# Kernel tuning notes

Measured on AMD Instinct MI355X. Metric: run time of the kernel, lower is better.

The kernel has to match this reference:

```python
import jax, jax.numpy as jnp
import numpy as np

ELEM, EMBD, WIN = 128, 128, 128

def setup_inputs() -> dict:
    key = jax.random.key(0)
    ks = jax.random.split(key, 7)
    s = 1.0 / np.sqrt(ELEM)
    return {
        "x": jax.random.normal(ks[0], (8, 16384, ELEM), dtype=jnp.float32),
        "Wq": jax.random.uniform(ks[1], (EMBD, ELEM), jnp.float32, -s, s),
        "bq": jax.random.uniform(ks[2], (EMBD,), jnp.float32, -s, s),
        "Wk": jax.random.uniform(ks[3], (EMBD, ELEM), jnp.float32, -s, s),
        "bk": jax.random.uniform(ks[4], (EMBD,), jnp.float32, -s, s),
        "Wv": jax.random.uniform(ks[5], (EMBD, ELEM), jnp.float32, -s, s),
        "bv": jax.random.uniform(ks[6], (EMBD,), jnp.float32, -s, s),
    }

def reference(x, Wq, bq, Wk, bk, Wv, bv):
    N, S, E = x.shape
    P = S // WIN
    xp = x.reshape(N, P, WIN, E)  # [N,P,W,E]
    q = jnp.einsum('npwe,de->npwd', xp, Wq) + bq
    k = jnp.einsum('npwe,de->npwd', xp, Wk) + bk
    v = jnp.einsum('npwe,de->npwd', xp, Wv) + bv
    # note: original applies NO 1/sqrt(d) scaling
    scores = jnp.einsum('npwd,npud->npwu', q, k)  # [N,P,W,W]
    attn = jax.nn.softmax(scores, axis=-1)
    out = jnp.einsum('npwu,npud->npwd', attn, v)
    return out.reshape(N, S, EMBD)
```

## Files before the change

kernel.cpp:

```cpp
#include <hip/hip_runtime.h>

#define LDSP 136

typedef _Float16 h8 __attribute__((ext_vector_type(8)));
typedef _Float16 h4 __attribute__((ext_vector_type(4)));
typedef float    f4 __attribute__((ext_vector_type(4)));
typedef float    fx16 __attribute__((ext_vector_type(16)));
typedef unsigned u32x4 __attribute__((ext_vector_type(4)));

union VF { u32x4 u; h8 h; };

__device__ __forceinline__ void bar_lds() {
    asm volatile("s_waitcnt lgkmcnt(0)" ::: "memory");
    __builtin_amdgcn_s_barrier();
    __builtin_amdgcn_sched_barrier(0);
}

__device__ __forceinline__ unsigned pkh(float a, float b) {
    union { _Float16 h[2]; unsigned u; } t;
    t.h[0] = (_Float16)a; t.h[1] = (_Float16)b;
    return t.u;
}

__global__ void prep(const float* __restrict__ Wq, const float* __restrict__ Wk,
                     const float* __restrict__ bq, const float* __restrict__ Wv,
                     _Float16* __restrict__ Mt, _Float16* __restrict__ Wvh,
                     float* __restrict__ ck) {
    int idx = blockIdx.x * 256 + threadIdx.x;
    int e = idx & 127, f = idx >> 7;
    float a0 = 0.f, a1 = 0.f, a2 = 0.f, a3 = 0.f;
    for (int d = 0; d < 128; d += 4) {
        a0 += Wk[(d + 0) * 128 + f] * Wq[(d + 0) * 128 + e];
        a1 += Wk[(d + 1) * 128 + f] * Wq[(d + 1) * 128 + e];
        a2 += Wk[(d + 2) * 128 + f] * Wq[(d + 2) * 128 + e];
        a3 += Wk[(d + 3) * 128 + f] * Wq[(d + 3) * 128 + e];
    }
    Mt[idx]  = (_Float16)((a0 + a1) + (a2 + a3));
    Wvh[idx] = (_Float16)Wv[idx];

    if (blockIdx.x == 0 && threadIdx.x < 128) {
        int t = threadIdx.x;
        float c0 = 0.f, c1 = 0.f, c2 = 0.f, c3 = 0.f;
        for (int d = 0; d < 128; d += 4) {
            c0 += bq[d + 0] * Wk[(d + 0) * 128 + t];
            c1 += bq[d + 1] * Wk[(d + 1) * 128 + t];
            c2 += bq[d + 2] * Wk[(d + 2) * 128 + t];
            c3 += bq[d + 3] * Wk[(d + 3) * 128 + t];
        }
        ck[t] = (c0 + c1) + (c2 + c3);
    }
}

__global__ __launch_bounds__(512, 4) void attn(
    const float* __restrict__ x, const _Float16* __restrict__ Mt,
    const _Float16* __restrict__ Wvh, const float* __restrict__ ck,
    const float* __restrict__ bv, float* __restrict__ out) {
    __shared__ _Float16 Xs[128 * LDSP];
    __shared__ _Float16 Ts[128 * LDSP];
    __shared__ float2   Sm[256];

    const int tid  = threadIdx.x;
    const int wv   = tid >> 6;
    const int lane = tid & 63;
    const int l32  = lane & 31;
    const int hi   = lane >> 5;
    const int hv   = wv & 1;
    const int t4   = wv >> 1;

    const size_t base = (size_t)blockIdx.x * (128 * 128);

#pragma unroll
    for (int j = 0; j < 8; ++j) {
        int idx = 4 * tid + 2048 * j;
        int row = idx >> 7, col = idx & 127;
        f4 f = *(const f4*)(x + base + idx);
        h4 h = {(_Float16)f.x, (_Float16)f.y, (_Float16)f.z, (_Float16)f.w};
        *(h4*)(&Xs[row * LDSP + col]) = h;
    }
    bar_lds();

    const float bvv = bv[t4 * 32 + l32];

    VF vfr[8];
    {
        fx16 av0, av1, av2, av3;
#pragma unroll
        for (int r = 0; r < 16; ++r) av0[r] = bvv;
        av1 = av0; av2 = av0; av3 = av0;
#pragma unroll
        for (int e0 = 0; e0 < 8; ++e0) {
            h8 wf = *(const h8*)(Wvh + (t4 * 32 + l32) * 128 + e0 * 16 + hi * 8);
            h8 x0 = *(const h8*)(&Xs[( 0 + l32) * LDSP + e0 * 16 + hi * 8]);
            h8 x1 = *(const h8*)(&Xs[(32 + l32) * LDSP + e0 * 16 + hi * 8]);
            h8 x2 = *(const h8*)(&Xs[(64 + l32) * LDSP + e0 * 16 + hi * 8]);
            h8 x3 = *(const h8*)(&Xs[(96 + l32) * LDSP + e0 * 16 + hi * 8]);
            av0 = __builtin_amdgcn_mfma_f32_32x32x16_f16(x0, wf, av0, 0, 0, 0);
            av1 = __builtin_amdgcn_mfma_f32_32x32x16_f16(x1, wf, av1, 0, 0, 0);
            av2 = __builtin_amdgcn_mfma_f32_32x32x16_f16(x2, wf, av2, 0, 0, 0);
            av3 = __builtin_amdgcn_mfma_f32_32x32x16_f16(x3, wf, av3, 0, 0, 0);
        }
#define PACK_TILE(av, T) {                                                        \
        unsigned A0 = pkh(av[0], av[1]),  A1 = pkh(av[2], av[3]);                 \
        unsigned B0 = pkh(av[4], av[5]),  B1 = pkh(av[6], av[7]);                 \
        unsigned C0 = pkh(av[8], av[9]),  C1 = pkh(av[10], av[11]);               \
        unsigned D0 = pkh(av[12], av[13]), D1 = pkh(av[14], av[15]);              \
        asm volatile("v_permlane32_swap_b32 %0, %1" : "+v"(A0), "+v"(B0));        \
        asm volatile("v_permlane32_swap_b32 %0, %1" : "+v"(A1), "+v"(B1));        \
        asm volatile("v_permlane32_swap_b32 %0, %1" : "+v"(C0), "+v"(D0));        \
        asm volatile("v_permlane32_swap_b32 %0, %1" : "+v"(C1), "+v"(D1));        \
        vfr[2 * T].u     = (u32x4){A0, A1, B0, B1};                               \
        vfr[2 * T + 1].u = (u32x4){C0, C1, D0, D1};                               \
    }
        PACK_TILE(av0, 0) PACK_TILE(av1, 1) PACK_TILE(av2, 2) PACK_TILE(av3, 3)
#undef PACK_TILE
    }

    {
        fx16 accT0, accT1;
        {
            f4 ckv[4];
#pragma unroll
            for (int run = 0; run < 4; ++run)
                ckv[run] = *(const f4*)(ck + t4 * 32 + run * 8 + 4 * hi);
#pragma unroll
            for (int r = 0; r < 16; ++r) accT0[r] = ckv[r >> 2][r & 3];
            accT1 = accT0;
        }
#pragma unroll
        for (int e0 = 0; e0 < 8; ++e0) {
            h8 mt = *(const h8*)(Mt + (t4 * 32 + l32) * 128 + e0 * 16 + hi * 8);
            h8 b0 = *(const h8*)(&Xs[(hv * 64 + l32) * LDSP + e0 * 16 + hi * 8]);
            h8 b1 = *(const h8*)(&Xs[(hv * 64 + 32 + l32) * LDSP + e0 * 16 + hi * 8]);
            accT0 = __builtin_amdgcn_mfma_f32_32x32x16_f16(mt, b0, accT0, 0, 0, 0);
            accT1 = __builtin_amdgcn_mfma_f32_32x32x16_f16(mt, b1, accT1, 0, 0, 0);
        }
#pragma unroll
        for (int run = 0; run < 4; ++run) {
            h4 h0 = {(_Float16)accT0[run * 4 + 0], (_Float16)accT0[run * 4 + 1],
                     (_Float16)accT0[run * 4 + 2], (_Float16)accT0[run * 4 + 3]};
            *(h4*)(&Ts[(hv * 64 + l32) * LDSP + t4 * 32 + run * 8 + 4 * hi]) = h0;
            h4 h1 = {(_Float16)accT1[run * 4 + 0], (_Float16)accT1[run * 4 + 1],
                     (_Float16)accT1[run * 4 + 2], (_Float16)accT1[run * 4 + 3]};
            *(h4*)(&Ts[(hv * 64 + 32 + l32) * LDSP + t4 * 32 + run * 8 + 4 * hi]) = h1;
        }
    }
    bar_lds();

    fx16 s0, s1;
#pragma unroll
    for (int r = 0; r < 16; ++r) s0[r] = 0.f;
    s1 = s0;
#pragma unroll
    for (int f0 = 0; f0 < 8; ++f0) {
        h8 tf = *(const h8*)(&Ts[(t4 * 32 + l32) * LDSP + f0 * 16 + hi * 8]);
        h8 a0 = *(const h8*)(&Xs[(hv * 64 + l32) * LDSP + f0 * 16 + hi * 8]);
        h8 a1 = *(const h8*)(&Xs[(hv * 64 + 32 + l32) * LDSP + f0 * 16 + hi * 8]);
        s0 = __builtin_amdgcn_mfma_f32_32x32x16_f16(a0, tf, s0, 0, 0, 0);
        s1 = __builtin_amdgcn_mfma_f32_32x32x16_f16(a1, tf, s1, 0, 0, 0);
    }
    float m = -1e30f;
#pragma unroll
    for (int r = 0; r < 16; ++r) m = fmaxf(m, fmaxf(s0[r], s1[r]));
    m = fmaxf(m, __shfl_xor(m, 32, 64));
    float ss = 0.f;
#pragma unroll
    for (int r = 0; r < 16; ++r) {
        s0[r] = __expf(s0[r] - m);
        s1[r] = __expf(s1[r] - m);
        ss += s0[r] + s1[r];
    }
    ss += __shfl_xor(ss, 32, 64);
    if (hi == 0) Sm[hv * 128 + t4 * 32 + l32] = make_float2(m, ss);
    bar_lds();
    float2 om = Sm[(hv ^ 1) * 128 + t4 * 32 + l32];
    float M   = fmaxf(m, om.x);
    float inv = __expf(m - M) / (ss * __expf(m - M) + om.y * __expf(om.x - M));
#pragma unroll
    for (int run = 0; run < 4; ++run) {
        h4 p0 = {(_Float16)(s0[run * 4 + 0] * inv), (_Float16)(s0[run * 4 + 1] * inv),
                 (_Float16)(s0[run * 4 + 2] * inv), (_Float16)(s0[run * 4 + 3] * inv)};
        *(h4*)(&Ts[(t4 * 32 + l32) * LDSP + hv * 64 + run * 8 + 4 * hi]) = p0;
        h4 p1 = {(_Float16)(s1[run * 4 + 0] * inv), (_Float16)(s1[run * 4 + 1] * inv),
                 (_Float16)(s1[run * 4 + 2] * inv), (_Float16)(s1[run * 4 + 3] * inv)};
        *(h4*)(&Ts[(t4 * 32 + l32) * LDSP + hv * 64 + 32 + run * 8 + 4 * hi]) = p1;
    }
    bar_lds();

    fx16 o0, o1;
#pragma unroll
    for (int r = 0; r < 16; ++r) o0[r] = 0.f;
    o1 = o0;
#pragma unroll
    for (int us = 0; us < 8; ++us) {
        h8 p0 = *(const h8*)(&Ts[(hv * 32 + l32) * LDSP + us * 16 + hi * 8]);
        h8 p1 = *(const h8*)(&Ts[((2 + hv) * 32 + l32) * LDSP + us * 16 + hi * 8]);
        o0 = __builtin_amdgcn_mfma_f32_32x32x16_f16(p0, vfr[us].h, o0, 0, 0, 0);
        o1 = __builtin_amdgcn_mfma_f32_32x32x16_f16(p1, vfr[us].h, o1, 0, 0, 0);
    }
    float* ob = out + base;
#pragma unroll
    for (int r = 0; r < 16; ++r) {
        int wrow = (r & 3) + 8 * (r >> 2) + 4 * hi;
        ob[(size_t)(hv * 32 + wrow) * 128 + t4 * 32 + l32]       = o0[r];
        ob[(size_t)((2 + hv) * 32 + wrow) * 128 + t4 * 32 + l32] = o1[r];
    }
}

extern "C" void kernel_launch(void* const* d_in, const int* in_sizes, int n_in,
                              void* d_out, int out_size, void* d_ws, size_t ws_size,
                              hipStream_t stream) {
    const float* x  = (const float*)d_in[0];
    const float* Wq = (const float*)d_in[1];
    const float* bq = (const float*)d_in[2];
    const float* Wk = (const float*)d_in[3];
    const float* Wv = (const float*)d_in[5];
    const float* bv = (const float*)d_in[6];

    _Float16* Mt  = (_Float16*)d_ws;
    _Float16* Wvh = Mt + 16384;
    float*    ckp = (float*)(Wvh + 16384);

    prep<<<64, 256, 0, stream>>>(Wq, Wk, bq, Wv, Mt, Wvh, ckp);
    attn<<<1024, 512, 0, stream>>>(x, Mt, Wvh, ckp, bv, (float*)d_out);
}
```

Before: 146.5 us.

## Process four windows per block with register prefetch and in-register softmax

Each block now loops over four consecutive windows. It double-buffers the converted x tile in LDS and prefetches the next window's x into registers while the current one is computed. The wave decomposition changes so each wave owns whole score rows. Softmax then needs no cross-wave LDS reduction, and the T and P operands stay in registers via permlane packing, with V transposed into LDS instead. This removes barriers and LDS round trips, but the two waves sharing a row tile both compute the same projected-key and score tiles. The grid also shrinks to 256 blocks with launch bounds lowered to 2 blocks per SM.

```diff
diff --git a/kernel.cpp b/kernel.cpp
--- a/kernel.cpp
+++ b/kernel.cpp
@@ -20,6 +20,19 @@
     union { _Float16 h[2]; unsigned u; } t;
     t.h[0] = (_Float16)a; t.h[1] = (_Float16)b;
     return t.u;
+}
+
+#define PACK_TILE(av, out0, out1) {                                           \
+    unsigned A0 = pkh(av[0], av[1]),   A1 = pkh(av[2], av[3]);                \
+    unsigned B0 = pkh(av[4], av[5]),   B1 = pkh(av[6], av[7]);                \
+    unsigned C0 = pkh(av[8], av[9]),   C1 = pkh(av[10], av[11]);              \
+    unsigned D0 = pkh(av[12], av[13]), D1 = pkh(av[14], av[15]);              \
+    asm volatile("v_permlane32_swap_b32 %0, %1" : "+v"(A0), "+v"(B0));        \
+    asm volatile("v_permlane32_swap_b32 %0, %1" : "+v"(A1), "+v"(B1));        \
+    asm volatile("v_permlane32_swap_b32 %0, %1" : "+v"(C0), "+v"(D0));        \
+    asm volatile("v_permlane32_swap_b32 %0, %1" : "+v"(C1), "+v"(D1));        \
+    (out0).u = (u32x4){A0, A1, B0, B1};                                       \
+    (out1).u = (u32x4){C0, C1, D0, D1};                                       \
 }
 
 __global__ void prep(const float* __restrict__ Wq, const float* __restrict__ Wk,
@@ -51,158 +64,161 @@
     }
 }
 
-__global__ __launch_bounds__(512, 4) void attn(
+__global__ __launch_bounds__(512, 2) void attn(
     const float* __restrict__ x, const _Float16* __restrict__ Mt,
     const _Float16* __restrict__ Wvh, const float* __restrict__ ck,
     const float* __restrict__ bv, float* __restrict__ out) {
-    __shared__ _Float16 Xs[128 * LDSP];
-    __shared__ _Float16 Ts[128 * LDSP];
-    __shared__ float2   Sm[256];
+    __shared__ _Float16 Xs[2][128 * LDSP];
+    __shared__ _Float16 Vs[128 * LDSP];
 
     const int tid  = threadIdx.x;
     const int wv   = tid >> 6;
     const int lane = tid & 63;
     const int l32  = lane & 31;
     const int hi   = lane >> 5;
-    const int hv   = wv & 1;
-    const int t4   = wv >> 1;
-
-    const size_t base = (size_t)blockIdx.x * (128 * 128);
-
-#pragma unroll
-    for (int j = 0; j < 8; ++j) {
-        int idx = 4 * tid + 2048 * j;
-        int row = idx >> 7, col = idx & 127;
-        f4 f = *(const f4*)(x + base + idx);
-        h4 h = {(_Float16)f.x, (_Float16)f.y, (_Float16)f.z, (_Float16)f.w};
-        *(h4*)(&Xs[row * LDSP + col]) = h;
-    }
-    bar_lds();
-
-    const float bvv = bv[t4 * 32 + l32];
-
-    VF vfr[8];
-    {
-        fx16 av0, av1, av2, av3;
-#pragma unroll
-        for (int r = 0; r < 16; ++r) av0[r] = bvv;
-        av1 = av0; av2 = av0; av3 = av0;
-#pragma unroll
-        for (int e0 = 0; e0 < 8; ++e0) {
-            h8 wf = *(const h8*)(Wvh + (t4 * 32 + l32) * 128 + e0 * 16 + hi * 8);
-            h8 x0 = *(const h8*)(&Xs[( 0 + l32) * LDSP + e0 * 16 + hi * 8]);
-            h8 x1 = *(const h8*)(&Xs[(32 + l32) * LDSP + e0 * 16 + hi * 8]);
-            h8 x2 = *(const h8*)(&Xs[(64 + l32) * LDSP + e0 * 16 + hi * 8]);
-            h8 x3 = *(const h8*)(&Xs[(96 + l32) * LDSP + e0 * 16 + hi * 8]);
-            av0 = __builtin_amdgcn_mfma_f32_32x32x16_f16(x0, wf, av0, 0, 0, 0);
-            av1 = __builtin_amdgcn_mfma_f32_32x32x16_f16(x1, wf, av1, 0, 0, 0);
-            av2 = __builtin_amdgcn_mfma_f32_32x32x16_f16(x2, wf, av2, 0, 0, 0);
-            av3 = __builtin_amdgcn_mfma_f32_32x32x16_f16(x3, wf, av3, 0, 0, 0);
-        }
-#define PACK_TILE(av, T) {                                                        \
-        unsigned A0 = pkh(av[0], av[1]),  A1 = pkh(av[2], av[3]);                 \
-        unsigned B0 = pkh(av[4], av[5]),  B1 = pkh(av[6], av[7]);                 \
-        unsigned C0 = pkh(av[8], av[9]),  C1 = pkh(av[10], av[11]);               \
-        unsigned D0 = pkh(av[12], av[13]), D1 = pkh(av[14], av[15]);              \
-        asm volatile("v_permlane32_swap_b32 %0, %1" : "+v"(A0), "+v"(B0));        \
-        asm volatile("v_permlane32_swap_b32 %0, %1" : "+v"(A1), "+v"(B1));        \
-        asm volatile("v_permlane32_swap_b32 %0, %1" : "+v"(C0), "+v"(D0));        \
-        asm volatile("v_permlane32_swap_b32 %0, %1" : "+v"(C1), "+v"(D1));        \
-        vfr[2 * T].u     = (u32x4){A0, A1, B0, B1};                               \
-        vfr[2 * T + 1].u = (u32x4){C0, C1, D0, D1};                               \
-    }
-        PACK_TILE(av0, 0) PACK_TILE(av1, 1) PACK_TILE(av2, 2) PACK_TILE(av3, 3)
-#undef PACK_TILE
-    }
-
-    {
-        fx16 accT0, accT1;
+    const int wt   = wv >> 1;
+    const int ph   = wv & 1;
+
+    const float bvv = bv[wt * 32 + l32];
+    const size_t base0 = (size_t)blockIdx.x * 4 * (128 * 128);
+
+    f4 pf[8];
+#pragma unroll
+    for (int j = 0; j < 8; ++j)
+        pf[j] = *(const f4*)(x + base0 + 4 * tid + 2048 * j);
+
+    for (int it = 0; it < 4; ++it) {
+        _Float16* X = Xs[it & 1];
+
+#pragma unroll
+        for (int j = 0; j < 8; ++j) {
+            int idx = 4 * tid + 2048 * j;
+            int row = idx >> 7, col = idx & 127;
+            f4 f = pf[j];
+            h4 h = {(_Float16)f.x, (_Float16)f.y, (_Float16)f.z, (_Float16)f.w};
+            *(h4*)(&X[row * LDSP + col]) = h;
+        }
+        if (it < 3) {
+            const float* nx = x + base0 + (size_t)(it + 1) * (128 * 128);
+#pragma unroll
+            for (int j = 0; j < 8; ++j)
+                pf[j] = *(const f4*)(nx + 4 * tid + 2048 * j);
+        }
+        bar_lds();
+
         {
-            f4 ckv[4];
-#pragma unroll
-            for (int run = 0; run < 4; ++run)
-                ckv[run] = *(const f4*)(ck + t4 * 32 + run * 8 + 4 * hi);
-#pragma unroll
-            for (int r = 0; r < 16; ++r) accT0[r] = ckv[r >> 2][r & 3];
-            accT1 = accT0;
-        }
-#pragma unroll
-        for (int e0 = 0; e0 < 8; ++e0) {
-            h8 mt = *(const h8*)(Mt + (t4 * 32 + l32) * 128 + e0 * 16 + hi * 8);
-            h8 b0 = *(const h8*)(&Xs[(hv * 64 + l32) * LDSP + e0 * 16 + hi * 8]);
-            h8 b1 = *(const h8*)(&Xs[(hv * 64 + 32 + l32) * LDSP + e0 * 16 + hi * 8]);
-            accT0 = __builtin_amdgcn_mfma_f32_32x32x16_f16(mt, b0, accT0, 0, 0, 0);
-            accT1 = __builtin_amdgcn_mfma_f32_32x32x16_f16(mt, b1, accT1, 0, 0, 0);
-        }
-#pragma unroll
-        for (int run = 0; run < 4; ++run) {
-            h4 h0 = {(_Float16)accT0[run * 4 + 0], (_Float16)accT0[run * 4 + 1],
-                     (_Float16)accT0[run * 4 + 2], (_Float16)accT0[run * 4 + 3]};
-            *(h4*)(&Ts[(hv * 64 + l32) * LDSP + t4 * 32 + run * 8 + 4 * hi]) = h0;
-            h4 h1 = {(_Float16)accT1[run * 4 + 0], (_Float16)accT1[run * 4 + 1],
-                     (_Float16)accT1[run * 4 + 2], (_Float16)accT1[run * 4 + 3]};
-            *(h4*)(&Ts[(hv * 64 + 32 + l32) * LDSP + t4 * 32 + run * 8 + 4 * hi]) = h1;
-        }
-    }
-    bar_lds();
-
-    fx16 s0, s1;
-#pragma unroll
-    for (int r = 0; r < 16; ++r) s0[r] = 0.f;
-    s1 = s0;
-#pragma unroll
-    for (int f0 = 0; f0 < 8; ++f0) {
-        h8 tf = *(const h8*)(&Ts[(t4 * 32 + l32) * LDSP + f0 * 16 + hi * 8]);
-        h8 a0 = *(const h8*)(&Xs[(hv * 64 + l32) * LDSP + f0 * 16 + hi * 8]);
-        h8 a1 = *(const h8*)(&Xs[(hv * 64 + 32 + l32) * LDSP + f0 * 16 + hi * 8]);
-        s0 = __builtin_amdgcn_mfma_f32_32x32x16_f16(a0, tf, s0, 0, 0, 0);
-        s1 = __builtin_amdgcn_mfma_f32_32x32x16_f16(a1, tf, s1, 0, 0, 0);
-    }
-    float m = -1e30f;
-#pragma unroll
-    for (int r = 0; r < 16; ++r) m = fmaxf(m, fmaxf(s0[r], s1[r]));
-    m = fmaxf(m, __shfl_xor(m, 32, 64));
-    float ss = 0.f;
-#pragma unroll
-    for (int r = 0; r < 16; ++r) {
-        s0[r] = __expf(s0[r] - m);
-        s1[r] = __expf(s1[r] - m);
-        ss += s0[r] + s1[r];
-    }
-    ss += __shfl_xor(ss, 32, 64);
-    if (hi == 0) Sm[hv * 128 + t4 * 32 + l32] = make_float2(m, ss);
-    bar_lds();
-    float2 om = Sm[(hv ^ 1) * 128 + t4 * 32 + l32];
-    float M   = fmaxf(m, om.x);
-    float inv = __expf(m - M) / (ss * __expf(m - M) + om.y * __expf(om.x - M));
-#pragma unroll
-    for (int run = 0; run < 4; ++run) {
-        h4 p0 = {(_Float16)(s0[run * 4 + 0] * inv), (_Float16)(s0[run * 4 + 1] * inv),
-                 (_Float16)(s0[run * 4 + 2] * inv), (_Float16)(s0[run * 4 + 3] * inv)};
-        *(h4*)(&Ts[(t4 * 32 + l32) * LDSP + hv * 64 + run * 8 + 4 * hi]) = p0;
-        h4 p1 = {(_Float16)(s1[run * 4 + 0] * inv), (_Float16)(s1[run * 4 + 1] * inv),
-                 (_Float16)(s1[run * 4 + 2] * inv), (_Float16)(s1[run * 4 + 3] * inv)};
-        *(h4*)(&Ts[(t4 * 32 + l32) * LDSP + hv * 64 + 32 + run * 8 + 4 * hi]) = p1;
-    }
-    bar_lds();
-
-    fx16 o0, o1;
-#pragma unroll
-    for (int r = 0; r < 16; ++r) o0[r] = 0.f;
-    o1 = o0;
-#pragma unroll
-    for (int us = 0; us < 8; ++us) {
-        h8 p0 = *(const h8*)(&Ts[(hv * 32 + l32) * LDSP + us * 16 + hi * 8]);
-        h8 p1 = *(const h8*)(&Ts[((2 + hv) * 32 + l32) * LDSP + us * 16 + hi * 8]);
-        o0 = __builtin_amdgcn_mfma_f32_32x32x16_f16(p0, vfr[us].h, o0, 0, 0, 0);
-        o1 = __builtin_amdgcn_mfma_f32_32x32x16_f16(p1, vfr[us].h, o1, 0, 0, 0);
-    }
-    float* ob = out + base;
-#pragma unroll
-    for (int r = 0; r < 16; ++r) {
-        int wrow = (r & 3) + 8 * (r >> 2) + 4 * hi;
-        ob[(size_t)(hv * 32 + wrow) * 128 + t4 * 32 + l32]       = o0[r];
-        ob[(size_t)((2 + hv) * 32 + wrow) * 128 + t4 * 32 + l32] = o1[r];
+            fx16 av0, av1;
+#pragma unroll
+            for (int r = 0; r < 16; ++r) av0[r] = bvv;
+            av1 = av0;
+#pragma unroll
+            for (int e0 = 0; e0 < 8; ++e0) {
+                h8 wf = *(const h8*)(Wvh + (wt * 32 + l32) * 128 + e0 * 16 + hi * 8);
+                h8 x0 = *(const h8*)(&X[((2 * ph) * 32 + l32) * LDSP + e0 * 16 + hi * 8]);
+                h8 x1 = *(const h8*)(&X[((2 * ph + 1) * 32 + l32) * LDSP + e0 * 16 + hi * 8]);
+                av0 = __builtin_amdgcn_mfma_f32_32x32x16_f16(x0, wf, av0, 0, 0, 0);
+                av1 = __builtin_amdgcn_mfma_f32_32x32x16_f16(x1, wf, av1, 0, 0, 0);
+            }
+#pragma unroll
+            for (int run = 0; run < 4; ++run) {
+                h4 g0 = {(_Float16)av0[run * 4 + 0], (_Float16)av0[run * 4 + 1],
+                         (_Float16)av0[run * 4 + 2], (_Float16)av0[run * 4 + 3]};
+                *(h4*)(&Vs[(wt * 32 + l32) * LDSP + (2 * ph) * 32 + run * 8 + 4 * hi]) = g0;
+                h4 g1 = {(_Float16)av1[run * 4 + 0], (_Float16)av1[run * 4 + 1],
+                         (_Float16)av1[run * 4 + 2], (_Float16)av1[run * 4 + 3]};
+                *(h4*)(&Vs[(wt * 32 + l32) * LDSP + (2 * ph + 1) * 32 + run * 8 + 4 * hi]) = g1;
+            }
+        }
+
+        VF tfr[8];
+        {
+            h8 bx[8];
+#pragma unroll
+            for (int e0 = 0; e0 < 8; ++e0)
+                bx[e0] = *(const h8*)(&X[(wt * 32 + l32) * LDSP + e0 * 16 + hi * 8]);
+#pragma unroll
+            for (int ft = 0; ft < 4; ++ft) {
+                fx16 a;
+#pragma unroll
+                for (int run = 0; run < 4; ++run) {
+                    f4 c = *(const f4*)(ck + ft * 32 + run * 8 + 4 * hi);
+                    a[run * 4 + 0] = c.x; a[run * 4 + 1] = c.y;
+                    a[run * 4 + 2] = c.z; a[run * 4 + 3] = c.w;
+                }
+#pragma unroll
+                for (int e0 = 0; e0 < 8; ++e0) {
+                    h8 mt = *(const h8*)(Mt + (ft * 32 + l32) * 128 + e0 * 16 + hi * 8);
+                    a = __builtin_amdgcn_mfma_f32_32x32x16_f16(mt, bx[e0], a, 0, 0, 0);
+                }
+                PACK_TILE(a, tfr[2 * ft], tfr[2 * ft + 1]);
+            }
+        }
+        bar_lds();
+
+        fx16 su[4];
+#pragma unroll
+        for (int ut = 0; ut < 4; ++ut)
+#pragma unroll
+            for (int r = 0; r < 16; ++r) su[ut][r] = 0.f;
+#pragma unroll
+        for (int f0 = 0; f0 < 8; ++f0) {
+#pragma unroll
+            for (int ut = 0; ut < 4; ++ut) {
+                h8 ax = *(const h8*)(&X[(ut * 32 + l32) * LDSP + f0 * 16 + hi * 8]);
+                su[ut] = __builtin_amdgcn_mfma_f32_32x32x16_f16(ax, tfr[f0].h, su[ut], 0, 0, 0);
+            }
+        }
+
+        float m0 = -1e30f, m1 = -1e30f;
+#pragma unroll
+        for (int ut = 0; ut < 4; ++ut)
+#pragma unroll
+            for (int r = 0; r < 16; r += 2) {
+                m0 = fmaxf(m0, su[ut][r]);
+                m1 = fmaxf(m1, su[ut][r + 1]);
+            }
+        float m = fmaxf(m0, m1);
+        m = fmaxf(m, __shfl_xor(m, 32, 64));
+        float s0 = 0.f, s1 = 0.f;
+#pragma unroll
+        for (int ut = 0; ut < 4; ++ut)
+#pragma unroll
+            for (int r = 0; r < 16; r += 2) {
+                su[ut][r]     = __expf(su[ut][r] - m);
+                su[ut][r + 1] = __expf(su[ut][r + 1] - m);
+                s0 += su[ut][r];
+                s1 += su[ut][r + 1];
+            }
+        float ss = s0 + s1;
+        ss += __shfl_xor(ss, 32, 64);
+        float inv = 1.0f / ss;
+        VF pfr[8];
+#pragma unroll
+        for (int ut = 0; ut < 4; ++ut) {
+            fx16 p;
+#pragma unroll
+            for (int r = 0; r < 16; ++r) p[r] = su[ut][r] * inv;
+            PACK_TILE(p, pfr[2 * ut], pfr[2 * ut + 1]);
+        }
+
+        fx16 o0, o1;
+#pragma unroll
+        for (int r = 0; r < 16; ++r) o0[r] = 0.f;
+        o1 = o0;
+#pragma unroll
+        for (int u0 = 0; u0 < 8; ++u0) {
+            h8 v0 = *(const h8*)(&Vs[((2 * ph) * 32 + l32) * LDSP + u0 * 16 + hi * 8]);
+            h8 v1 = *(const h8*)(&Vs[((2 * ph + 1) * 32 + l32) * LDSP + u0 * 16 + hi * 8]);
+            o0 = __builtin_amdgcn_mfma_f32_32x32x16_f16(pfr[u0].h, v0, o0, 0, 0, 0);
+            o1 = __builtin_amdgcn_mfma_f32_32x32x16_f16(pfr[u0].h, v1, o1, 0, 0, 0);
+        }
+        float* ob = out + base0 + (size_t)it * (128 * 128);
+#pragma unroll
+        for (int r = 0; r < 16; ++r) {
+            int wrow = wt * 32 + (r & 3) + 8 * (r >> 2) + 4 * hi;
+            ob[(size_t)wrow * 128 + (2 * ph) * 32 + l32]     = o0[r];
+            ob[(size_t)wrow * 128 + (2 * ph + 1) * 32 + l32] = o1[r];
+        }
     }
 }
 
@@ -221,5 +237,5 @@
     float*    ckp = (float*)(Wvh + 16384);
 
     prep<<<64, 256, 0, stream>>>(Wq, Wk, bq, Wv, Mt, Wvh, ckp);
-    attn<<<1024, 512, 0, stream>>>(x, Mt, Wvh, ckp, bv, (float*)d_out);
-}
+    attn<<<256, 512, 0, stream>>>(x, Mt, Wvh, ckp, bv, (float*)d_out);
+}
```

New measurement: 174.9 us. 1.19x slower.
